# Optimization experiments

Measured on AMD Instinct MI355X. Metric: run time of the kernel, lower is better.

The kernel has to match this reference:

```python
import jax, jax.numpy as jnp
import numpy as np
from jax import lax

T, H, F, E, K = 4096, 1024, 2048, 8, 2

def setup_inputs() -> dict:
    key = jax.random.key(0)
    k1, k2, k3, k4 = jax.random.split(key, 4)
    return {
        "hidden_states": jax.random.normal(k1, (T, H), jnp.float32),
        "gate_w": jax.random.normal(k2, (E, H), jnp.float32) * 0.02,
        "w1": jax.random.normal(k3, (E, 2 * F, H), jnp.float32) * 0.02,  # fused gate+up
        "w2": jax.random.normal(k4, (E, H, F), jnp.float32) * 0.02,      # down proj
        "top_k": K,
    }

def reference(hidden_states, gate_w, w1, w2, top_k):
    tokens = hidden_states.shape[0]
    # Router gate (Linear, no bias)
    router_logits = hidden_states @ gate_w.T                     # [T, E]
    probs = jax.nn.softmax(router_logits.astype(jnp.float32), axis=-1)
    topk_w, topk_idx = lax.top_k(probs, top_k)                   # [T, K]
    topk_w = topk_w / jnp.sum(topk_w, axis=-1, keepdims=True)    # renormalize
    # Dense combine weights [T, E] (zero for unselected experts)
    combine = jnp.zeros_like(probs).at[jnp.arange(tokens)[:, None], topk_idx].add(topk_w)
    combine = combine.astype(hidden_states.dtype)

    def expert_step(acc, ew):
        w1_e, w2_e, c_e = ew                                     # [2F,H], [H,F], [T]
        h = hidden_states @ w1_e.T                               # [T, 2F]
        g, u = jnp.split(h, 2, axis=-1)
        y = (jax.nn.silu(g) * u) @ w2_e.T                        # [T, H]
        return acc + c_e[:, None] * y, None

    acc0 = jnp.zeros_like(hidden_states)
    final_hidden_states, _ = lax.scan(expert_step, acc0, (w1, w2, combine.T))
    return final_hidden_states, router_logits
```

## Files before the change

### kernel.cpp

```cpp
#include <hip/hip_runtime.h>

#define T 4096
#define Hdim 1024
#define Fdim 2048
#define NE 8
#define TOPK 2
#define TK (T*TOPK)

typedef unsigned short ushort_t;
typedef __attribute__((ext_vector_type(8))) short bf16x8;
typedef __attribute__((ext_vector_type(4))) float floatx4;

__device__ __forceinline__ ushort_t f2bf(float f) {
    unsigned u = __float_as_uint(f);
    u += 0x7fff + ((u >> 16) & 1);
    return (ushort_t)(u >> 16);
}
__device__ __forceinline__ uint4 cvt8(const float4 a, const float4 b) {
    uint4 r;
    r.x = (unsigned)f2bf(a.x) | ((unsigned)f2bf(a.y) << 16);
    r.y = (unsigned)f2bf(a.z) | ((unsigned)f2bf(a.w) << 16);
    r.z = (unsigned)f2bf(b.x) | ((unsigned)f2bf(b.y) << 16);
    r.w = (unsigned)f2bf(b.z) | ((unsigned)f2bf(b.w) << 16);
    return r;
}
__device__ __forceinline__ void gld16(const ushort_t* g, short* l) {
    __builtin_amdgcn_global_load_lds((const __attribute__((address_space(1))) void*)g,
                                     (__attribute__((address_space(3))) void*)l, 16, 0, 0);
}

__global__ __launch_bounds__(64) void router_kernel(
    const float* __restrict__ hs, const float* __restrict__ gw,
    float* __restrict__ logits_out, ushort_t* __restrict__ hsb,
    int2* __restrict__ choice, float2* __restrict__ cwt, int* __restrict__ counts)
{
    const int t = blockIdx.x;
    const int lane = threadIdx.x;
    if (t == 0 && lane < NE) counts[lane] = 0;

    float hreg[16];
#pragma unroll
    for (int i = 0; i < 16; ++i)
        hreg[i] = hs[(long)t * Hdim + lane + 64 * i];

#pragma unroll
    for (int i = 0; i < 16; ++i)
        hsb[(long)t * Hdim + lane + 64 * i] = f2bf(hreg[i]);

    float acc[NE];
#pragma unroll
    for (int e = 0; e < NE; ++e) {
        float s = 0.f;
#pragma unroll
        for (int i = 0; i < 16; ++i)
            s += hreg[i] * gw[e * Hdim + lane + 64 * i];
#pragma unroll
        for (int off = 32; off > 0; off >>= 1)
            s += __shfl_xor(s, off, 64);
        acc[e] = s;
    }

    if (lane < NE) logits_out[t * NE + lane] = acc[lane];

    if (lane == 0) {
        int i1 = 0;
#pragma unroll
        for (int e = 1; e < NE; ++e) if (acc[e] > acc[i1]) i1 = e;
        int i2 = -1;
#pragma unroll
        for (int e = 0; e < NE; ++e) {
            if (e == i1) continue;
            if (i2 < 0 || acc[e] > acc[i2]) i2 = e;
        }
        float p2 = __expf(acc[i2] - acc[i1]);
        float z  = 1.f + p2;
        choice[t] = make_int2(i1, i2);
        cwt[t]    = make_float2(1.f / z, p2 / z);
    }
}

__global__ __launch_bounds__(256) void scatter_kernel(
    const int2* __restrict__ choice, const float2* __restrict__ cwt,
    int* __restrict__ counts, int* __restrict__ tok_slot, float* __restrict__ tok_wt)
{
    __shared__ int lhist[NE];
    __shared__ int lbase[NE];
    __shared__ int lpos[NE];
    const int tid = threadIdx.x;
    if (tid < NE) { lhist[tid] = 0; lpos[tid] = 0; }
    __syncthreads();

    const int t = blockIdx.x * 256 + tid;
    int2   ch = choice[t];
    float2 wv = cwt[t];
    atomicAdd(&lhist[ch.x], 1);
    atomicAdd(&lhist[ch.y], 1);
    __syncthreads();

    if (tid < NE) lbase[tid] = atomicAdd(&counts[tid], lhist[tid]);
    __syncthreads();

    int p1 = atomicAdd(&lpos[ch.x], 1);
    int p2 = atomicAdd(&lpos[ch.y], 1);
    int o1 = lbase[ch.x] + p1;
    int o2 = lbase[ch.y] + p2;
    tok_slot[ch.x * T + o1] = t * TOPK + 0;
    tok_wt [ch.x * T + o1] = wv.x;
    tok_slot[ch.y * T + o2] = t * TOPK + 1;
    tok_wt [ch.y * T + o2] = wv.y;
}

__global__ __launch_bounds__(512, 3) void gemm1_kernel(
    const ushort_t* __restrict__ hsb, const float* __restrict__ w1,
    const int* __restrict__ counts, const int* __restrict__ tok_slot,
    ushort_t* __restrict__ actb)
{
    const int e = blockIdx.z;
    const int cnt = counts[e];
    const int row0 = blockIdx.y * 256;
    if (row0 >= cnt) return;
    const int f0 = blockIdx.x * 64;

    __shared__ short As[256 * 64];
    __shared__ short Bs[128 * 64];
    __shared__ int slotLds[256];

    const int tid = threadIdx.x;
    if (tid < 256) {
        int idx = row0 + tid;
        slotLds[tid] = (idx < cnt) ? tok_slot[e * T + idx] : -1;
    }
    __syncthreads();

    const ushort_t* srcA[4];
#pragma unroll
    for (int i = 0; i < 4; ++i) {
        int ci = i * 512 + tid;
        int r  = ci >> 3;
        int gc = (ci & 7) ^ (r & 7);
        int s  = slotLds[r];
        srcA[i] = hsb + (long)(s >= 0 ? (s >> 1) : 0) * Hdim + gc * 8;
    }
    const float* srcBf[2];
    int bDst[2];
#pragma unroll
    for (int i = 0; i < 2; ++i) {
        int ci = i * 512 + tid;
        int r  = ci >> 3;
        int gc = (ci & 7) ^ (r & 7);
        long frow = (r < 64) ? (long)(f0 + r) : (long)(Fdim + f0 + (r - 64));
        srcBf[i] = w1 + ((long)e * 2 * Fdim + frow) * Hdim + gc * 8;
        bDst[i]  = ci * 8;
    }

    const int lane = tid & 63;
    const int w = tid >> 6;
    const int wm = (w >> 1) * 64;
    const int wn = (w & 1) * 32;
    const int fr = lane & 15, fg = lane >> 4;
    const int cs0 = (fg ^ (fr & 7)) * 8;
    const int cs1 = ((4 + fg) ^ (fr & 7)) * 8;

    floatx4 accg[4][2] = {};
    floatx4 accu[4][2] = {};

    for (int k0 = 0; k0 < Hdim; k0 += 64) {
        __syncthreads();
#pragma unroll
        for (int i = 0; i < 4; ++i) gld16(srcA[i] + k0, &As[(i * 512 + tid) * 8]);
#pragma unroll
        for (int i = 0; i < 2; ++i) {
            float4 x = *(const float4*)(srcBf[i] + k0);
            float4 y = *(const float4*)(srcBf[i] + k0 + 4);
            *(uint4*)&Bs[bDst[i]] = cvt8(x, y);
        }
        __syncthreads();

#pragma unroll
        for (int kk = 0; kk < 2; ++kk) {
            const int cs = kk ? cs1 : cs0;
            bf16x8 a[4], g[2], u[2];
#pragma unroll
            for (int ms = 0; ms < 4; ++ms)
                a[ms] = *(const bf16x8*)&As[(wm + ms * 16 + fr) * 64 + cs];
#pragma unroll
            for (int ns = 0; ns < 2; ++ns) {
                g[ns] = *(const bf16x8*)&Bs[(wn + ns * 16 + fr) * 64 + cs];
                u[ns] = *(const bf16x8*)&Bs[(64 + wn + ns * 16 + fr) * 64 + cs];
            }
#pragma unroll
            for (int ms = 0; ms < 4; ++ms)
#pragma unroll
                for (int ns = 0; ns < 2; ++ns) {
                    accg[ms][ns] = __builtin_amdgcn_mfma_f32_16x16x32_bf16(a[ms], g[ns], accg[ms][ns], 0, 0, 0);
                    accu[ms][ns] = __builtin_amdgcn_mfma_f32_16x16x32_bf16(a[ms], u[ns], accu[ms][ns], 0, 0, 0);
                }
        }
    }

#pragma unroll
    for (int ms = 0; ms < 4; ++ms)
#pragma unroll
        for (int ns = 0; ns < 2; ++ns)
#pragma unroll
            for (int j = 0; j < 4; ++j) {
                int m = wm + ms * 16 + fg * 4 + j;
                int slot = slotLds[m];
                if (slot >= 0) {
                    int fcol = f0 + wn + ns * 16 + fr;
                    float gv = accg[ms][ns][j];
                    float uv = accu[ms][ns][j];
                    float av = (gv / (1.f + __expf(-gv))) * uv;
                    actb[(long)slot * Fdim + fcol] = f2bf(av);
                }
            }
}

__global__ __launch_bounds__(512, 4) void gemm2_kernel(
    const ushort_t* __restrict__ actb, const float* __restrict__ w2,
    const int* __restrict__ counts, const int* __restrict__ tok_slot,
    const float* __restrict__ tok_wt, float* __restrict__ partial)
{
    const int e = blockIdx.z;
    const int cnt = counts[e];
    const int row0 = blockIdx.y * 128;
    if (row0 >= cnt) return;
    const int h0 = blockIdx.x * 128;

    __shared__ short As[128 * 64];
    __shared__ short Bs[128 * 64];
    __shared__ int   slotLds[128];
    __shared__ float wtLds[128];

    const int tid = threadIdx.x;
    if (tid < 128) {
        int idx = row0 + tid;
        bool ok = idx < cnt;
        slotLds[tid] = ok ? tok_slot[e * T + idx] : -1;
        wtLds[tid]   = ok ? tok_wt [e * T + idx] : 0.f;
    }
    __syncthreads();

    const ushort_t* srcA[2];
#pragma unroll
    for (int i = 0; i < 2; ++i) {
        int ci = i * 512 + tid;
        int r  = ci >> 3;
        int gc = (ci & 7) ^ (r & 7);
        int s  = slotLds[r];
        srcA[i] = actb + (long)(s >= 0 ? s : 0) * Fdim + gc * 8;
    }
    const float* srcBf[2];
    int bDst[2];
#pragma unroll
    for (int i = 0; i < 2; ++i) {
        int ci = i * 512 + tid;
        int r  = ci >> 3;
        int gc = (ci & 7) ^ (r & 7);
        srcBf[i] = w2 + ((long)e * Hdim + (h0 + r)) * Fdim + gc * 8;
        bDst[i]  = ci * 8;
    }

    const int lane = tid & 63;
    const int w = tid >> 6;
    const int wm = (w >> 2) * 64;
    const int wn = (w & 3) * 32;
    const int fr = lane & 15, fg = lane >> 4;
    const int cs0 = (fg ^ (fr & 7)) * 8;
    const int cs1 = ((4 + fg) ^ (fr & 7)) * 8;

    floatx4 acc[4][2] = {};

    for (int k0 = 0; k0 < Fdim; k0 += 64) {
        __syncthreads();
#pragma unroll
        for (int i = 0; i < 2; ++i) gld16(srcA[i] + k0, &As[(i * 512 + tid) * 8]);
#pragma unroll
        for (int i = 0; i < 2; ++i) {
            float4 x = *(const float4*)(srcBf[i] + k0);
            float4 y = *(const float4*)(srcBf[i] + k0 + 4);
            *(uint4*)&Bs[bDst[i]] = cvt8(x, y);
        }
        __syncthreads();

#pragma unroll
        for (int kk = 0; kk < 2; ++kk) {
            const int cs = kk ? cs1 : cs0;
            bf16x8 a[4], b[2];
#pragma unroll
            for (int ms = 0; ms < 4; ++ms)
                a[ms] = *(const bf16x8*)&As[(wm + ms * 16 + fr) * 64 + cs];
#pragma unroll
            for (int ns = 0; ns < 2; ++ns)
                b[ns] = *(const bf16x8*)&Bs[(wn + ns * 16 + fr) * 64 + cs];
#pragma unroll
            for (int ms = 0; ms < 4; ++ms)
#pragma unroll
                for (int ns = 0; ns < 2; ++ns)
                    acc[ms][ns] = __builtin_amdgcn_mfma_f32_16x16x32_bf16(a[ms], b[ns], acc[ms][ns], 0, 0, 0);
        }
    }

#pragma unroll
    for (int ms = 0; ms < 4; ++ms)
#pragma unroll
        for (int ns = 0; ns < 2; ++ns)
#pragma unroll
            for (int j = 0; j < 4; ++j) {
                int m = wm + ms * 16 + fg * 4 + j;
                int slot = slotLds[m];
                if (slot >= 0) {
                    int hcol = h0 + wn + ns * 16 + fr;
                    partial[(long)slot * Hdim + hcol] = acc[ms][ns][j] * wtLds[m];
                }
            }
}

__global__ __launch_bounds__(256) void combine_kernel(
    const float* __restrict__ partial, float* __restrict__ out)
{
    long i = (long)blockIdx.x * 256 + threadIdx.x;
    int t  = (int)(i / (Hdim / 4));
    int h4 = (int)(i % (Hdim / 4));
    const float4 p0 = *(const float4*)&partial[(long)(2 * t    ) * Hdim + h4 * 4];
    const float4 p1 = *(const float4*)&partial[(long)(2 * t + 1) * Hdim + h4 * 4];
    float4 s;
    s.x = p0.x + p1.x; s.y = p0.y + p1.y; s.z = p0.z + p1.z; s.w = p0.w + p1.w;
    *(float4*)&out[(long)t * Hdim + h4 * 4] = s;
}

extern "C" void kernel_launch(void* const* d_in, const int* in_sizes, int n_in,
                              void* d_out, int out_size, void* d_ws, size_t ws_size,
                              hipStream_t stream)
{
    const float* hs = (const float*)d_in[0];
    const float* gw = (const float*)d_in[1];
    const float* w1 = (const float*)d_in[2];
    const float* w2 = (const float*)d_in[3];

    float* out        = (float*)d_out;
    float* logits_out = out + (long)T * Hdim;

    char* ws = (char*)d_ws;
    size_t off = 0;
    int* counts = (int*)(ws + off);          off += 256;
    int* tok_slot = (int*)(ws + off);        off += (size_t)NE * T * sizeof(int);
    float* tok_wt = (float*)(ws + off);      off += (size_t)NE * T * sizeof(float);
    off = (off + 255) & ~(size_t)255;
    ushort_t* hsb = (ushort_t*)(ws + off);   off += (size_t)T * Hdim * sizeof(ushort_t);
    off = (off + 255) & ~(size_t)255;
    ushort_t* actb = (ushort_t*)(ws + off);  off += (size_t)TK * Fdim * sizeof(ushort_t);
    off = (off + 255) & ~(size_t)255;
    float* partial = (float*)(ws + off);     off += (size_t)TK * Hdim * sizeof(float);
    int2*   choice = (int2*)actb;
    float2* cwt    = (float2*)((char*)actb + (size_t)T * sizeof(int2));

    router_kernel<<<T, 64, 0, stream>>>(hs, gw, logits_out, hsb, choice, cwt, counts);
    scatter_kernel<<<T / 256, 256, 0, stream>>>(choice, cwt, counts, tok_slot, tok_wt);
    gemm1_kernel<<<dim3(Fdim / 64, T / 256, NE), 512, 0, stream>>>(hsb, w1, counts, tok_slot, actb);
    gemm2_kernel<<<dim3(Hdim / 128, T / 128, NE), 512, 0, stream>>>(actb, w2, counts, tok_slot, tok_wt, partial);
    combine_kernel<<<(int)((long)T * Hdim / 4 / 256), 256, 0, stream>>>(partial, out);
}
```

Measured before the change: 450.3 us.

## Software-pipeline fp32 weight loads into registers across K-steps in both expert GEMMs

```diff
diff --git a/kernel.cpp b/kernel.cpp
--- a/kernel.cpp
+++ b/kernel.cpp
@@ -110,7 +110,39 @@
     tok_wt [ch.y * T + o2] = wv.y;
 }
 
-__global__ __launch_bounds__(512, 3) void gemm1_kernel(
+#define G1_LOADB(br, kof)                                              \
+    _Pragma("unroll")                                                  \
+    for (int i = 0; i < 2; ++i) {                                      \
+        br[2*i]   = *(const float4*)(srcBf[i] + (kof));                \
+        br[2*i+1] = *(const float4*)(srcBf[i] + (kof) + 4);            \
+    }
+#define G1_DSWRITE(br)                                                 \
+    _Pragma("unroll")                                                  \
+    for (int i = 0; i < 2; ++i)                                        \
+        *(uint4*)&Bs[bDst[i]] = cvt8(br[2*i], br[2*i+1]);
+#define G1_COMPUTE()                                                   \
+    _Pragma("unroll")                                                  \
+    for (int kk = 0; kk < 2; ++kk) {                                   \
+        const int cs = kk ? cs1 : cs0;                                 \
+        bf16x8 a[4], g[2], u[2];                                       \
+        _Pragma("unroll")                                              \
+        for (int ms = 0; ms < 4; ++ms)                                 \
+            a[ms] = *(const bf16x8*)&As[(wm + ms * 16 + fr) * 64 + cs];\
+        _Pragma("unroll")                                              \
+        for (int ns = 0; ns < 2; ++ns) {                               \
+            g[ns] = *(const bf16x8*)&Bs[(wn + ns * 16 + fr) * 64 + cs];\
+            u[ns] = *(const bf16x8*)&Bs[(64 + wn + ns * 16 + fr) * 64 + cs];\
+        }                                                              \
+        _Pragma("unroll")                                              \
+        for (int ms = 0; ms < 4; ++ms)                                 \
+            _Pragma("unroll")                                          \
+            for (int ns = 0; ns < 2; ++ns) {                           \
+                accg[ms][ns] = __builtin_amdgcn_mfma_f32_16x16x32_bf16(a[ms], g[ns], accg[ms][ns], 0, 0, 0); \
+                accu[ms][ns] = __builtin_amdgcn_mfma_f32_16x16x32_bf16(a[ms], u[ns], accu[ms][ns], 0, 0, 0); \
+            }                                                          \
+    }
+
+__global__ __launch_bounds__(512, 4) void gemm1_kernel(
     const ushort_t* __restrict__ hsb, const float* __restrict__ w1,
     const int* __restrict__ counts, const int* __restrict__ tok_slot,
     ushort_t* __restrict__ actb)
@@ -164,38 +196,42 @@
     floatx4 accg[4][2] = {};
     floatx4 accu[4][2] = {};
 
-    for (int k0 = 0; k0 < Hdim; k0 += 64) {
-        __syncthreads();
-#pragma unroll
-        for (int i = 0; i < 4; ++i) gld16(srcA[i] + k0, &As[(i * 512 + tid) * 8]);
-#pragma unroll
-        for (int i = 0; i < 2; ++i) {
-            float4 x = *(const float4*)(srcBf[i] + k0);
-            float4 y = *(const float4*)(srcBf[i] + k0 + 4);
-            *(uint4*)&Bs[bDst[i]] = cvt8(x, y);
+    float4 brE[4], brO[4];
+    G1_LOADB(brE, 0);
+
+    for (int t2 = 0; t2 < 8; ++t2) {
+        const int kE = 2 * t2 * 64;
+        const int kO = kE + 64;
+
+        if (t2) __builtin_amdgcn_s_barrier();
+        G1_DSWRITE(brE);
+#pragma unroll
+        for (int i = 0; i < 4; ++i) gld16(srcA[i] + kE, &As[(i * 512 + tid) * 8]);
+        __builtin_amdgcn_sched_barrier(0);
+        G1_LOADB(brO, kO);
+        asm volatile("s_waitcnt vmcnt(4) lgkmcnt(0)" ::: "memory");
+        __builtin_amdgcn_sched_barrier(0);
+        __builtin_amdgcn_s_barrier();
+        __builtin_amdgcn_s_setprio(1);
+        G1_COMPUTE();
+        __builtin_amdgcn_s_setprio(0);
+
+        __builtin_amdgcn_s_barrier();
+        G1_DSWRITE(brO);
+#pragma unroll
+        for (int i = 0; i < 4; ++i) gld16(srcA[i] + kO, &As[(i * 512 + tid) * 8]);
+        __builtin_amdgcn_sched_barrier(0);
+        if (t2 < 7) {
+            G1_LOADB(brE, kO + 64);
+            asm volatile("s_waitcnt vmcnt(4) lgkmcnt(0)" ::: "memory");
+        } else {
+            asm volatile("s_waitcnt vmcnt(0) lgkmcnt(0)" ::: "memory");
         }
-        __syncthreads();
-
-#pragma unroll
-        for (int kk = 0; kk < 2; ++kk) {
-            const int cs = kk ? cs1 : cs0;
-            bf16x8 a[4], g[2], u[2];
-#pragma unroll
-            for (int ms = 0; ms < 4; ++ms)
-                a[ms] = *(const bf16x8*)&As[(wm + ms * 16 + fr) * 64 + cs];
-#pragma unroll
-            for (int ns = 0; ns < 2; ++ns) {
-                g[ns] = *(const bf16x8*)&Bs[(wn + ns * 16 + fr) * 64 + cs];
-                u[ns] = *(const bf16x8*)&Bs[(64 + wn + ns * 16 + fr) * 64 + cs];
-            }
-#pragma unroll
-            for (int ms = 0; ms < 4; ++ms)
-#pragma unroll
-                for (int ns = 0; ns < 2; ++ns) {
-                    accg[ms][ns] = __builtin_amdgcn_mfma_f32_16x16x32_bf16(a[ms], g[ns], accg[ms][ns], 0, 0, 0);
-                    accu[ms][ns] = __builtin_amdgcn_mfma_f32_16x16x32_bf16(a[ms], u[ns], accu[ms][ns], 0, 0, 0);
-                }
-        }
+        __builtin_amdgcn_sched_barrier(0);
+        __builtin_amdgcn_s_barrier();
+        __builtin_amdgcn_s_setprio(1);
+        G1_COMPUTE();
+        __builtin_amdgcn_s_setprio(0);
     }
 
 #pragma unroll
@@ -216,6 +252,34 @@
             }
 }
 
+#define G2_LOADB(br, kof)                                              \
+    _Pragma("unroll")                                                  \
+    for (int i = 0; i < 2; ++i) {                                      \
+        br[2*i]   = *(const float4*)(srcBf[i] + (kof));                \
+        br[2*i+1] = *(const float4*)(srcBf[i] + (kof) + 4);            \
+    }
+#define G2_DSWRITE(br)                                                 \
+    _Pragma("unroll")                                                  \
+    for (int i = 0; i < 2; ++i)                                        \
+        *(uint4*)&Bs[bDst[i]] = cvt8(br[2*i], br[2*i+1]);
+#define G2_COMPUTE()                                                   \
+    _Pragma("unroll")                                                  \
+    for (int kk = 0; kk < 2; ++kk) {                                   \
+        const int cs = kk ? cs1 : cs0;                                 \
+        bf16x8 a[4], b[2];                                             \
+        _Pragma("unroll")                                              \
+        for (int ms = 0; ms < 4; ++ms)                                 \
+            a[ms] = *(const bf16x8*)&As[(wm + ms * 16 + fr) * 64 + cs];\
+        _Pragma("unroll")                                              \
+        for (int ns = 0; ns < 2; ++ns)                                 \
+            b[ns] = *(const bf16x8*)&Bs[(wn + ns * 16 + fr) * 64 + cs];\
+        _Pragma("unroll")                                              \
+        for (int ms = 0; ms < 4; ++ms)                                 \
+            _Pragma("unroll")                                          \
+            for (int ns = 0; ns < 2; ++ns)                             \
+                acc[ms][ns] = __builtin_amdgcn_mfma_f32_16x16x32_bf16(a[ms], b[ns], acc[ms][ns], 0, 0, 0); \
+    }
+
 __global__ __launch_bounds__(512, 4) void gemm2_kernel(
     const ushort_t* __restrict__ actb, const float* __restrict__ w2,
     const int* __restrict__ counts, const int* __restrict__ tok_slot,
@@ -271,34 +335,42 @@
 
     floatx4 acc[4][2] = {};
 
-    for (int k0 = 0; k0 < Fdim; k0 += 64) {
-        __syncthreads();
-#pragma unroll
-        for (int i = 0; i < 2; ++i) gld16(srcA[i] + k0, &As[(i * 512 + tid) * 8]);
-#pragma unroll
-        for (int i = 0; i < 2; ++i) {
-            float4 x = *(const float4*)(srcBf[i] + k0);
-            float4 y = *(const float4*)(srcBf[i] + k0 + 4);
-            *(uint4*)&Bs[bDst[i]] = cvt8(x, y);
+    float4 brE[4], brO[4];
+    G2_LOADB(brE, 0);
+
+    for (int t2 = 0; t2 < 16; ++t2) {
+        const int kE = 2 * t2 * 64;
+        const int kO = kE + 64;
+
+        if (t2) __builtin_amdgcn_s_barrier();
+        G2_DSWRITE(brE);
+#pragma unroll
+        for (int i = 0; i < 2; ++i) gld16(srcA[i] + kE, &As[(i * 512 + tid) * 8]);
+        __builtin_amdgcn_sched_barrier(0);
+        G2_LOADB(brO, kO);
+        asm volatile("s_waitcnt vmcnt(4) lgkmcnt(0)" ::: "memory");
+        __builtin_amdgcn_sched_barrier(0);
+        __builtin_amdgcn_s_barrier();
+        __builtin_amdgcn_s_setprio(1);
+        G2_COMPUTE();
+        __builtin_amdgcn_s_setprio(0);
+
+        __builtin_amdgcn_s_barrier();
+        G2_DSWRITE(brO);
+#pragma unroll
+        for (int i = 0; i < 2; ++i) gld16(srcA[i] + kO, &As[(i * 512 + tid) * 8]);
+        __builtin_amdgcn_sched_barrier(0);
+        if (t2 < 15) {
+            G2_LOADB(brE, kO + 64);
+            asm volatile("s_waitcnt vmcnt(4) lgkmcnt(0)" ::: "memory");
+        } else {
+            asm volatile("s_waitcnt vmcnt(0) lgkmcnt(0)" ::: "memory");
         }
-        __syncthreads();
-
-#pragma unroll
-        for (int kk = 0; kk < 2; ++kk) {
-            const int cs = kk ? cs1 : cs0;
-            bf16x8 a[4], b[2];
-#pragma unroll
-            for (int ms = 0; ms < 4; ++ms)
-                a[ms] = *(const bf16x8*)&As[(wm + ms * 16 + fr) * 64 + cs];
-#pragma unroll
-            for (int ns = 0; ns < 2; ++ns)
-                b[ns] = *(const bf16x8*)&Bs[(wn + ns * 16 + fr) * 64 + cs];
-#pragma unroll
-            for (int ms = 0; ms < 4; ++ms)
-#pragma unroll
-                for (int ns = 0; ns < 2; ++ns)
-                    acc[ms][ns] = __builtin_amdgcn_mfma_f32_16x16x32_bf16(a[ms], b[ns], acc[ms][ns], 0, 0, 0);
-        }
+        __builtin_amdgcn_sched_barrier(0);
+        __builtin_amdgcn_s_barrier();
+        __builtin_amdgcn_s_setprio(1);
+        G2_COMPUTE();
+        __builtin_amdgcn_s_setprio(0);
     }
 
 #pragma unroll
```

Result: slower. 492.1 us (+9.3%).
